# Performance work log

Hardware: AMD Instinct MI355X
Metric: run time of the kernel (lower is better)

Reference implementation:

```python
import jax, jax.numpy as jnp
import numpy as np

K_GF = 8      # neighbors used by graph filtering
EPS = 1e-5    # BatchNorm eps
B, CW, SD, M = 32, 512, 16, 2048


def _conv1x1(x, w, b):
    # x: [B, Cin, M], w: [Cout, Cin], b: [Cout]
    return jnp.einsum('oi,bim->bom', w, x) + b[None, :, None]


def _bn(x, g, be):
    # training-mode BatchNorm1d over (batch, points)
    mu = jnp.mean(x, axis=(0, 2), keepdims=True)
    var = jnp.var(x, axis=(0, 2), keepdims=True)
    return g[None, :, None] * (x - mu) * jax.lax.rsqrt(var + EPS) + be[None, :, None]


def _graph_filtering(x):
    # x: [B, 3, M]  -> sharpening filter over kNN graph: out = 2*x - mean(neighbors)
    pts = jnp.transpose(x, (0, 2, 1))                      # [B, M, 3]
    sq = jnp.sum(pts * pts, axis=-1)                       # [B, M]
    d = sq[:, :, None] + sq[:, None, :] - 2.0 * jnp.einsum('bmc,bnc->bmn', pts, pts)
    idx = jax.lax.top_k(-d, K_GF + 1)[1][..., 1:]          # [B, M, K] drop self
    neigh = jax.vmap(lambda p, i: p[i])(pts, idx)          # [B, M, K, 3]
    out = 2.0 * pts - jnp.mean(neigh, axis=2)
    return jnp.transpose(out, (0, 2, 1))


def setup_inputs() -> dict:
    key = jax.random.key(0)
    ks = jax.random.split(key, 12)
    def w(k, o, i):
        return jax.random.normal(k, (o, i), jnp.float32) * (1.0 / np.sqrt(i))
    h = [256, CW, 512, 256, 128, 64]
    inp = {
        'z': jax.random.normal(ks[0], (B, CW), jnp.float32),
        's': jax.random.normal(ks[1], (B, SD, M), jnp.float32),
        'w_m1': w(ks[2], h[0], SD), 'b_m1': jnp.zeros((h[0],), jnp.float32),
        'w_m2': w(ks[3], h[1], h[0]), 'b_m2': jnp.zeros((h[1],), jnp.float32),
        'w_out': w(ks[4], 3, h[5]), 'b_out': jnp.zeros((3,), jnp.float32),
    }
    for j, (ci, co) in enumerate(zip(h[1:-1], h[2:])):
        inp[f'w_c{j}'] = w(ks[5 + j], co, ci)
        inp[f'b_c{j}'] = jnp.zeros((co,), jnp.float32)
        inp[f'g_c{j}'] = jnp.ones((co,), jnp.float32)
        inp[f'be_c{j}'] = jnp.zeros((co,), jnp.float32)
    return inp


def reference(z, s, w_m1, b_m1, w_m2, b_m2, w_out, b_out,
              w_c0, b_c0, g_c0, be_c0, w_c1, b_c1, g_c1, be_c1,
              w_c2, b_c2, g_c2, be_c2, w_c3, b_c3, g_c3, be_c3):
    x = s / jnp.linalg.norm(s, axis=1, keepdims=True)          # unit samples
    x = jax.nn.relu(_conv1x1(x, w_m1, b_m1))                   # map_samples1
    x = jnp.clip(_conv1x1(x, w_m2, b_m2), -1.0, 1.0)           # map_samples2 (Hardtanh)
    x = z[:, :, None] * x                                      # z-modulation
    for w_, b_, g_, be_ in ((w_c0, b_c0, g_c0, be_c0), (w_c1, b_c1, g_c1, be_c1),
                            (w_c2, b_c2, g_c2, be_c2), (w_c3, b_c3, g_c3, be_c3)):
        x = jax.nn.relu(_bn(_conv1x1(x, w_, b_), g_, be_))
    x = _conv1x1(x, w_out, b_out)                              # [B, 3, M]
    return _graph_filtering(x)
```

## Files before the change

kernel.cpp:

```cpp
#include <hip/hip_runtime.h>
#include <math.h>

#define Bn 32
#define Mn 2048
#define Nn 65536
#define Hn 32768
#define SDn 16
#define CWn 512
#define EPSf 1e-5f
#define KGF 8
#define WTOT 573440
#define LSC 2048.0f
#define LSCI (1.0f / 2048.0f)

typedef unsigned short u16;
typedef _Float16 fp16_t;
typedef __attribute__((ext_vector_type(8))) _Float16 h8v;
typedef __attribute__((ext_vector_type(4))) float f4v;

__device__ __forceinline__ u16 f2h(float f) {
    union { fp16_t h; u16 u; } c; c.h = (fp16_t)f; return c.u;
}
__device__ __forceinline__ float h2f(u16 u) {
    union { fp16_t h; u16 u; } c; c.u = u; return (float)c.h;
}
__device__ __forceinline__ void fsplit(float f, u16& hi, u16& lo) {
    hi = f2h(f);
    lo = f2h((f - h2f(hi)) * LSC);
}
__device__ __forceinline__ float fjoin(u16 hi, u16 lo) {
    return h2f(hi) + h2f(lo) * LSCI;
}
__device__ __forceinline__ void gll16(const u16* g, u16* l) {
    __builtin_amdgcn_global_load_lds((const __attribute__((address_space(1))) void*)g,
                                     (__attribute__((address_space(3))) void*)l, 16, 0, 0);
}
__device__ __forceinline__ unsigned umin(unsigned a, unsigned b) { return a < b ? a : b; }
__device__ __forceinline__ unsigned umax(unsigned a, unsigned b) { return a > b ? a : b; }

__global__ __launch_bounds__(256) void prep_kernel(
    const float* __restrict__ wm1, const float* __restrict__ wm2,
    const float* __restrict__ wc0, const float* __restrict__ wc1,
    const float* __restrict__ wc2, const float* __restrict__ wc3,
    const float* __restrict__ s,
    u16* __restrict__ wbuf, u16* __restrict__ xs, float* __restrict__ stats)
{
    const int bid = blockIdx.x;
    const int tid = threadIdx.x;
    if (bid < 2240) {
        int i = bid * 256 + tid;
        float w; int r, k, Cin; size_t base;
        if (i < 8192) {
            r = i >> 5; k = i & 31; Cin = 32; base = 0;
            w = (k < SDn) ? wm1[r * SDn + k] : 0.f;
        } else {
            int j = i - 8192;
            if (j < 131072)                    { r = j >> 8; k = j & 255; Cin = 256; base = 16384;   w = wm2[j]; }
            else if ((j -= 131072) < 262144)   { r = j >> 9; k = j & 511; Cin = 512; base = 278528;  w = wc0[j]; }
            else if ((j -= 262144) < 131072)   { r = j >> 9; k = j & 511; Cin = 512; base = 802816;  w = wc1[j]; }
            else if ((j -= 131072) < 32768)    { r = j >> 8; k = j & 255; Cin = 256; base = 1064960; w = wc2[j]; }
            else { j -= 32768;                   r = j >> 7; k = j & 127; Cin = 128; base = 1130496; w = wc3[j]; }
        }
        const size_t addr = base + (size_t)r * (2 * Cin) + k;
        u16 hi, lo; fsplit(w, hi, lo);
        wbuf[addr] = hi;
        wbuf[addr + Cin] = lo;
    } else if (bid < 2496) {
        const int b2 = bid - 2240;
        const int m = (b2 & 7) * 256 + tid;
        const int b = b2 >> 3;
        const float* sp = s + (size_t)b * SDn * Mn + m;
        float v[SDn]; float sq = 0.f;
#pragma unroll
        for (int c = 0; c < SDn; ++c) { v[c] = sp[(size_t)c * Mn]; sq += v[c] * v[c]; }
        const float r = 1.0f / sqrtf(sq);
        unsigned int uh[8], ul[8];
#pragma unroll
        for (int c = 0; c < 8; ++c) {
            u16 h0, l0, h1, l1;
            fsplit(v[2 * c] * r, h0, l0);
            fsplit(v[2 * c + 1] * r, h1, l1);
            uh[c] = (unsigned int)h0 | ((unsigned int)h1 << 16);
            ul[c] = (unsigned int)l0 | ((unsigned int)l1 << 16);
        }
        uint4* xp = (uint4*)(xs + (size_t)(b * Mn + m) * 64);
        xp[0] = make_uint4(uh[0], uh[1], uh[2], uh[3]);
        xp[1] = make_uint4(uh[4], uh[5], uh[6], uh[7]);
        xp[2] = make_uint4(0, 0, 0, 0);
        xp[3] = make_uint4(0, 0, 0, 0);
        xp[4] = make_uint4(ul[0], ul[1], ul[2], ul[3]);
        xp[5] = make_uint4(ul[4], ul[5], ul[6], ul[7]);
        xp[6] = make_uint4(0, 0, 0, 0);
        xp[7] = make_uint4(0, 0, 0, 0);
    } else {
        float4 z4 = {0.f, 0.f, 0.f, 0.f};
        float4* sp4 = (float4*)stats;
#pragma unroll
        for (int k = 0; k < 4; ++k) sp4[tid * 4 + k] = z4;
    }
}

template<int RW, int CWv, int EPI, int MY, int IBN, int CINT, int NT>
__global__ __launch_bounds__(NT) void mfma_gemm(
    const u16* __restrict__ W, const u16* __restrict__ X, u16* __restrict__ Y,
    const float* __restrict__ bias, const float* __restrict__ zmod,
    const float* __restrict__ statsIn, const float* __restrict__ gin,
    const float* __restrict__ bein, float* __restrict__ stats, int Cout)
{
    static_assert(NT == RW * CWv * 64, "wave grid must exactly cover the tile");
    constexpr int BM = RW * 64, BN = CWv * 64;
    constexpr int ASEG = (BM * 4) / NT;
    constexpr int BSEG = (BN * 4) / NT;
    constexpr int LMY = (MY == 1) ? 0 : (MY == 2) ? 1 : (MY == 4) ? 2 : 3;
    constexpr int SW = 2 * CINT;
    constexpr int NST = CINT >> 5;
    constexpr int VMSTEP = 2 * ASEG + 2 * BSEG;
    constexpr int SSTATN = (EPI == 2) ? (CWv * BM * 2) : 1;
    constexpr int BNN = IBN ? (CINT * 2) : 1;
    constexpr int AUXN = (SSTATN > BNN) ? SSTATN : BNN;
    constexpr int BSTR = 2 * BM + 8;
    constexpr int BROWS = CWv * 16;
    constexpr int UNITS = BROWS * 2 * (BM / 8);
    static_assert(UNITS % NT == 0, "store units must tile the block");
    __shared__ __align__(16) u16 Ah[2][BM * 32], Al[2][BM * 32];
    __shared__ __align__(16) u16 Bh[2][BN * 32], Bl[2][BN * 32];
    __shared__ __align__(16) u16 bounce[BROWS * BSTR];
    __shared__ float saux[AUXN];

    const int tid = threadIdx.x;
    const int wave = tid >> 6;
    const int lane = tid & 63;
    const int wm = wave & (RW - 1), wn = wave / RW;
    const int l15 = lane & 15, q = lane >> 4;
    const int lin = blockIdx.x;
    const int xcd = lin & 7;
    const int jj = lin >> 3;
    const int m0 = (jj & (MY - 1)) * BM;
    const int n0 = (xcd + ((jj >> LMY) << 3)) * BN;

    f4v acc0[4][4], accL[4][4];
#pragma unroll
    for (int i = 0; i < 4; ++i)
#pragma unroll
        for (int j = 0; j < 4; ++j) {
            acc0[i][j] = (f4v){0.f, 0.f, 0.f, 0.f};
            accL[i][j] = (f4v){0.f, 0.f, 0.f, 0.f};
        }

    auto stageAB = [&](int ks, int buf) {
        const int k0 = ks << 5;
#pragma unroll
        for (int s = 0; s < ASEG; ++s) {
            const int flat = s * NT + tid;
            const int row = flat >> 2;
            const int qs = (flat & 3) ^ ((row >> 1) & 3);
            const u16* ga = W + (size_t)(m0 + row) * SW + k0 + qs * 8;
            gll16(ga, Ah[buf] + flat * 8);
            gll16(ga + CINT, Al[buf] + flat * 8);
        }
#pragma unroll
        for (int s = 0; s < BSEG; ++s) {
            const int flat = s * NT + tid;
            const int row = flat >> 2;
            const int qs = (flat & 3) ^ ((row >> 1) & 3);
            const u16* gb = X + (size_t)(n0 + row) * SW + k0 + qs * 8;
            gll16(gb, Bh[buf] + flat * 8);
            gll16(gb + CINT, Bl[buf] + flat * 8);
        }
    };

    if constexpr (IBN) {
        const float inv = 1.0f / (float)Nn;
        for (int c = tid; c < CINT; c += NT) {
            const float mean = statsIn[c * 2] * inv;
            const float var = statsIn[c * 2 + 1] * inv - mean * mean;
            const float sc = gin[c] / sqrtf(var + EPSf);
            saux[c * 2] = sc;
            saux[c * 2 + 1] = fmaf(-mean, sc, bein[c]);
        }
        asm volatile("s_waitcnt vmcnt(0) lgkmcnt(0)" ::: "memory");
    }
    stageAB(0, 0);
    if constexpr (NST > 1) stageAB(1, 1);

#pragma unroll 1
    for (int ks = 0; ks < NST; ++ks) {
        const int cur = ks & 1;
        if (ks + 1 < NST) {
            asm volatile("s_waitcnt vmcnt(%0)" :: "n"(VMSTEP) : "memory");
        } else {
            asm volatile("s_waitcnt vmcnt(0)" ::: "memory");
        }
        __builtin_amdgcn_s_barrier();
        __builtin_amdgcn_sched_barrier(0);
        h8v afh[4], afl[4], bfh[4], bfl[4];
#pragma unroll
        for (int i = 0; i < 4; ++i) {
            const int ar = wm * 64 + i * 16 + l15;
            const int ao = ar * 32 + ((q ^ ((ar >> 1) & 3)) << 3);
            afh[i] = *(const h8v*)(Ah[cur] + ao);
            afl[i] = *(const h8v*)(Al[cur] + ao);
        }
#pragma unroll
        for (int j = 0; j < 4; ++j) {
            const int br = wn * 64 + j * 16 + l15;
            const int bo = br * 32 + ((q ^ ((br >> 1) & 3)) << 3);
            bfh[j] = *(const h8v*)(Bh[cur] + bo);
            bfl[j] = *(const h8v*)(Bl[cur] + bo);
        }
        if constexpr (IBN) {
            const int kb = ((ks << 5) + q * 8) * 2;
            const float4 p0 = *(const float4*)(saux + kb);
            const float4 p1 = *(const float4*)(saux + kb + 4);
            const float4 p2 = *(const float4*)(saux + kb + 8);
            const float4 p3 = *(const float4*)(saux + kb + 12);
            const float sc8[8] = {p0.x, p0.z, p1.x, p1.z, p2.x, p2.z, p3.x, p3.z};
            const float sh8[8] = {p0.y, p0.w, p1.y, p1.w, p2.y, p2.w, p3.y, p3.w};
#pragma unroll
            for (int j = 0; j < 4; ++j) {
#pragma unroll
                for (int e = 0; e < 8; ++e) {
                    const float v = (float)bfh[j][e] + (float)bfl[j][e] * LSCI;
                    const float a = fmaxf(fmaf(v, sc8[e], sh8[e]), 0.f);
                    const fp16_t hh = (fp16_t)a;
                    bfh[j][e] = hh;
                    bfl[j][e] = (fp16_t)((a - (float)hh) * LSC);
                }
            }
        }
        __builtin_amdgcn_s_setprio(1);
#pragma unroll
        for (int i = 0; i < 4; ++i)
#pragma unroll
            for (int j = 0; j < 4; ++j)
                accL[i][j] = __builtin_amdgcn_mfma_f32_16x16x32_f16(afh[i], bfl[j], accL[i][j], 0, 0, 0);
#pragma unroll
        for (int i = 0; i < 4; ++i)
#pragma unroll
            for (int j = 0; j < 4; ++j)
                acc0[i][j] = __builtin_amdgcn_mfma_f32_16x16x32_f16(afh[i], bfh[j], acc0[i][j], 0, 0, 0);
#pragma unroll
        for (int i = 0; i < 4; ++i)
#pragma unroll
            for (int j = 0; j < 4; ++j)
                accL[i][j] = __builtin_amdgcn_mfma_f32_16x16x32_f16(afl[i], bfh[j], accL[i][j], 0, 0, 0);
        __builtin_amdgcn_s_setprio(0);
        __builtin_amdgcn_s_barrier();
        if (ks + 2 < NST) stageAB(ks + 2, cur);
    }

    float* sstat = saux;
    const int bb = n0 >> 11;
    const int SY = 2 * Cout;
    float ssum[4][4], ssq[4][4];
    if constexpr (EPI == 2) {
#pragma unroll
        for (int i = 0; i < 4; ++i)
#pragma unroll
            for (int r = 0; r < 4; ++r) { ssum[i][r] = 0.f; ssq[i][r] = 0.f; }
    }
    const int nl_w = wn * 16 + l15;
#pragma unroll
    for (int j = 0; j < 4; ++j) {
        __builtin_amdgcn_s_barrier();
#pragma unroll
        for (int i = 0; i < 4; ++i) {
            const int chb = m0 + wm * 64 + i * 16 + q * 4;
            const float4 bias4 = *(const float4*)(bias + chb);
            float v0 = fmaf(accL[i][j][0], LSCI, acc0[i][j][0]) + bias4.x;
            float v1 = fmaf(accL[i][j][1], LSCI, acc0[i][j][1]) + bias4.y;
            float v2 = fmaf(accL[i][j][2], LSCI, acc0[i][j][2]) + bias4.z;
            float v3 = fmaf(accL[i][j][3], LSCI, acc0[i][j][3]) + bias4.w;
            if constexpr (EPI == 0) {
                v0 = fmaxf(v0, 0.f); v1 = fmaxf(v1, 0.f); v2 = fmaxf(v2, 0.f); v3 = fmaxf(v3, 0.f);
            } else if constexpr (EPI == 1) {
                const float4 z4 = *(const float4*)(zmod + bb * CWn + chb);
                v0 = fminf(fmaxf(v0, -1.f), 1.f) * z4.x;
                v1 = fminf(fmaxf(v1, -1.f), 1.f) * z4.y;
                v2 = fminf(fmaxf(v2, -1.f), 1.f) * z4.z;
                v3 = fminf(fmaxf(v3, -1.f), 1.f) * z4.w;
            } else {
                ssum[i][0] += v0; ssum[i][1] += v1; ssum[i][2] += v2; ssum[i][3] += v3;
                ssq[i][0] += v0 * v0; ssq[i][1] += v1 * v1; ssq[i][2] += v2 * v2; ssq[i][3] += v3 * v3;
            }
            u16 h0, l0, h1, l1, h2, l2, h3, l3;
            fsplit(v0, h0, l0); fsplit(v1, h1, l1);
            fsplit(v2, h2, l2); fsplit(v3, h3, l3);
            const ushort4 hv = {h0, h1, h2, h3};
            const ushort4 lv = {l0, l1, l2, l3};
            const int chl = wm * 64 + i * 16 + q * 4;
            *(ushort4*)(bounce + nl_w * BSTR + chl) = hv;
            *(ushort4*)(bounce + nl_w * BSTR + BM + chl) = lv;
        }
        __builtin_amdgcn_s_barrier();
#pragma unroll
        for (int u0 = 0; u0 < UNITS; u0 += NT) {
            const int u = u0 + tid;
            const int nl = u / (2 * (BM / 8));
            const int rem = u % (2 * (BM / 8));
            const int plane = rem / (BM / 8);
            const int off8 = rem % (BM / 8);
            const int n = n0 + (nl >> 4) * 64 + j * 16 + (nl & 15);
            u16* yp = Y + (size_t)n * SY + (plane ? Cout : 0) + m0 + off8 * 8;
            *(uint4*)yp = *(const uint4*)(bounce + nl * BSTR + plane * BM + off8 * 8);
        }
    }
    if constexpr (EPI == 2) {
#pragma unroll
        for (int i = 0; i < 4; ++i) {
#pragma unroll
            for (int r = 0; r < 4; ++r) {
#pragma unroll
                for (int d = 1; d < 16; d <<= 1) {
                    ssum[i][r] += __shfl_xor(ssum[i][r], d);
                    ssq[i][r]  += __shfl_xor(ssq[i][r], d);
                }
            }
            if (l15 == 0) {
                const int chl = wm * 64 + i * 16 + q * 4;
#pragma unroll
                for (int r = 0; r < 4; ++r) {
                    sstat[(wn * BM + chl + r) * 2]     = ssum[i][r];
                    sstat[(wn * BM + chl + r) * 2 + 1] = ssq[i][r];
                }
            }
        }
        __syncthreads();
        if (tid < BM) {
            float s0 = 0.f, s1 = 0.f;
#pragma unroll
            for (int w = 0; w < CWv; ++w) {
                s0 += sstat[(w * BM + tid) * 2];
                s1 += sstat[(w * BM + tid) * 2 + 1];
            }
            atomicAdd(&stats[(m0 + tid) * 2], s0);
            atomicAdd(&stats[(m0 + tid) * 2 + 1], s1);
        }
    }
}

__global__ __launch_bounds__(256) void finalconv_pm(
    const u16* __restrict__ y3, const float* __restrict__ statsIn,
    const float* __restrict__ gin, const float* __restrict__ bein,
    const float* __restrict__ wout, const float* __restrict__ bout,
    float* __restrict__ pts)
{
    __shared__ float swo[3][64];
    __shared__ float ssc[64], ssh[64];
    const int tid = threadIdx.x;
    if (tid < 192) swo[tid / 64][tid % 64] = wout[tid];
    if (tid < 64) {
        const float inv = 1.0f / (float)Nn;
        const float mean = statsIn[tid * 2] * inv;
        const float var = statsIn[tid * 2 + 1] * inv - mean * mean;
        const float sc = gin[tid] / sqrtf(var + EPSf);
        ssc[tid] = sc;
        ssh[tid] = fmaf(-mean, sc, bein[tid]);
    }
    __syncthreads();
    const int n = blockIdx.x * 256 + tid;
    const uint4* yph = (const uint4*)(y3 + (size_t)n * 128);
    float d0 = bout[0], d1 = bout[1], d2 = bout[2];
#pragma unroll
    for (int cc = 0; cc < 8; ++cc) {
        const uint4 H = yph[cc];
        const uint4 L = yph[8 + cc];
        const unsigned hu[4] = {H.x, H.y, H.z, H.w};
        const unsigned lu[4] = {L.x, L.y, L.z, L.w};
#pragma unroll
        for (int e = 0; e < 4; ++e) {
            const int c = cc * 8 + e * 2;
            const float v0 = fjoin((u16)(hu[e] & 0xffff), (u16)(lu[e] & 0xffff));
            const float v1 = fjoin((u16)(hu[e] >> 16), (u16)(lu[e] >> 16));
            const float a0 = fmaxf(fmaf(v0, ssc[c], ssh[c]), 0.f);
            const float a1 = fmaxf(fmaf(v1, ssc[c + 1], ssh[c + 1]), 0.f);
            d0 = fmaf(a0, swo[0][c], d0); d0 = fmaf(a1, swo[0][c + 1], d0);
            d1 = fmaf(a0, swo[1][c], d1); d1 = fmaf(a1, swo[1][c + 1], d1);
            d2 = fmaf(a0, swo[2][c], d2); d2 = fmaf(a1, swo[2][c + 1], d2);
        }
    }
    float4 p = {d0, d1, d2, d0 * d0 + d1 * d1 + d2 * d2};
    *(float4*)(pts + (size_t)n * 4) = p;
}

__global__ __launch_bounds__(512) void knn_kernel(const float* __restrict__ pts,
                                                  float* __restrict__ out) {
    __shared__ __align__(16) float4 sp[Mn];
    const int b = blockIdx.y;
    const int tid = threadIdx.x;
    const float4* pb = (const float4*)pts + (size_t)b * Mn;
    for (int i = tid; i < Mn; i += 512) sp[i] = pb[i];
    __syncthreads();
    const int lane = tid & 63;
    const int wv = tid >> 6;
    const int seg = lane & 15;
    const int ptl = (wv << 2) | (lane >> 4);
    const int m = blockIdx.x * 32 + ptl;
    const float4 p = sp[m];
    const int cself = (seg == (m >> 7)) ? (m & 127) : 128;
    const int nb = seg << 7;
    unsigned bk[8];
#pragma unroll
    for (int k = 0; k < 8; ++k) bk[k] = 0xFFFFFFFFu;
    for (int t = 0; t < 128; ++t) {
        const int tt = (t + seg) & 127;
        const float4 q = sp[nb | tt];
        const float dot = fmaf(p.x, q.x, fmaf(p.y, q.y, p.z * q.z));
        float d = fmaf(-2.f, dot, q.w + p.w);
        d = fmaxf(d, 0.f);
        unsigned key = (__float_as_uint(d) & 0xFFFFFF80u) | (unsigned)tt;
        key = (tt == cself) ? 0xFFFFFFFFu : key;
        bk[7] = umin(bk[7], key);
#pragma unroll
        for (int k = 6; k >= 0; --k) {
            const unsigned lo = umin(bk[k], bk[k + 1]);
            bk[k + 1] = umax(bk[k], bk[k + 1]);
            bk[k] = lo;
        }
    }
    unsigned ok[8];
#pragma unroll
    for (int k = 0; k < 8; ++k) ok[k] = bk[k];
#pragma unroll
    for (int r = 1; r <= 8; r <<= 1) {
        unsigned od[8], md[8];
#pragma unroll
        for (int k = 0; k < 8; ++k) od[k] = (unsigned)__shfl_xor((int)bk[k], r);
#pragma unroll
        for (int k = 0; k < 8; ++k) md[k] = umin(bk[k], od[7 - k]);
#define CSU(a, c) { const unsigned lo_ = umin(md[a], md[c]); md[c] = umax(md[a], md[c]); md[a] = lo_; }
        CSU(0,4); CSU(1,5); CSU(2,6); CSU(3,7);
        CSU(0,2); CSU(1,3); CSU(4,6); CSU(5,7);
        CSU(0,1); CSU(2,3); CSU(4,5); CSU(6,7);
#undef CSU
#pragma unroll
        for (int k = 0; k < 8; ++k) bk[k] = md[k];
    }
    const unsigned TK = bk[7];
    float slt[4] = {0.f, 0.f, 0.f, 0.f};
    float seq[4] = {0.f, 0.f, 0.f, 0.f};
#pragma unroll
    for (int k = 0; k < 8; ++k) {
        const unsigned key = ok[k];
        const float4 q = sp[nb | (int)(key & 127u)];
        const bool lt = key < TK;
        const bool eq = key == TK;
        slt[0] += lt ? q.x : 0.f; slt[1] += lt ? q.y : 0.f;
        slt[2] += lt ? q.z : 0.f; slt[3] += lt ? 1.f : 0.f;
        seq[0] += eq ? q.x : 0.f; seq[1] += eq ? q.y : 0.f;
        seq[2] += eq ? q.z : 0.f; seq[3] += eq ? 1.f : 0.f;
    }
#pragma unroll
    for (int r = 1; r <= 8; r <<= 1) {
#pragma unroll
        for (int k = 0; k < 4; ++k) {
            slt[k] += __shfl_xor(slt[k], r);
            seq[k] += __shfl_xor(seq[k], r);
        }
    }
    if (seg == 0) {
        const float scale = (8.f - slt[3]) / seq[3];
        const float nx = fmaf(scale, seq[0], slt[0]);
        const float ny = fmaf(scale, seq[1], slt[1]);
        const float nz = fmaf(scale, seq[2], slt[2]);
        const float s8 = 0.125f;
        float* ob = out + (size_t)b * 3 * Mn;
        ob[m]          = 2.f * p.x - nx * s8;
        ob[Mn + m]     = 2.f * p.y - ny * s8;
        ob[2 * Mn + m] = 2.f * p.z - nz * s8;
    }
}

extern "C" void kernel_launch(void* const* d_in, const int* in_sizes, int n_in,
                              void* d_out, int out_size, void* d_ws, size_t ws_size,
                              hipStream_t stream)
{
    (void)in_sizes; (void)n_in; (void)out_size;
    const float* z     = (const float*)d_in[0];
    const float* s     = (const float*)d_in[1];
    const float* w_m1  = (const float*)d_in[2];
    const float* b_m1  = (const float*)d_in[3];
    const float* w_m2  = (const float*)d_in[4];
    const float* b_m2  = (const float*)d_in[5];
    const float* w_out = (const float*)d_in[6];
    const float* b_out = (const float*)d_in[7];
    const float* w_c[4]  = {(const float*)d_in[8],  (const float*)d_in[12], (const float*)d_in[16], (const float*)d_in[20]};
    const float* b_c[4]  = {(const float*)d_in[9],  (const float*)d_in[13], (const float*)d_in[17], (const float*)d_in[21]};
    const float* g_c[4]  = {(const float*)d_in[10], (const float*)d_in[14], (const float*)d_in[18], (const float*)d_in[22]};
    const float* be_c[4] = {(const float*)d_in[11], (const float*)d_in[15], (const float*)d_in[19], (const float*)d_in[23]};

    char* ws = (char*)d_ws;
    const size_t MB = 1024ull * 1024ull;
    float* outp = (float*)d_out;
    if (ws_size < 208 * MB) return;

    u16*   wbuf  = (u16*)ws;
    float* stats = (float*)(ws + 3 * MB);
    u16*   xs  = (u16*)(ws + 4 * MB);
    u16*   x1  = (u16*)(ws + 12 * MB);
    u16*   x2  = (u16*)(ws + 76 * MB);
    u16*   y0  = (u16*)(ws + 12 * MB);
    u16*   y0a = (u16*)(ws + 12 * MB);
    u16*   y0b = (u16*)(ws + 76 * MB);
    u16*   y1  = (u16*)(ws + 140 * MB);
    u16*   y2  = (u16*)(ws + 12 * MB);
    u16*   y3  = (u16*)(ws + 76 * MB);
    float* pts = (float*)(ws + 4 * MB);

    prep_kernel<<<2497, 256, 0, stream>>>(w_m1, w_m2, w_c[0], w_c[1], w_c[2], w_c[3], s, wbuf, xs, stats);
    mfma_gemm<2, 2, 0, 2, 0, 32, 256><<<1024, 256, 0, stream>>>(wbuf, xs, x1, b_m1, nullptr, nullptr, nullptr, nullptr, nullptr, 256);
    mfma_gemm<4, 2, 1, 2, 0, 256, 512><<<1024, 512, 0, stream>>>(wbuf + 16384, x1, x2, b_m2, z, nullptr, nullptr, nullptr, nullptr, 512);
    mfma_gemm<4, 2, 2, 2, 0, 512, 512><<<512, 512, 0, stream>>>(wbuf + 278528, x2, y0a, b_c[0], nullptr, nullptr, nullptr, nullptr, stats + 0, 512);
    mfma_gemm<4, 2, 2, 2, 0, 512, 512><<<512, 512, 0, stream>>>(wbuf + 278528, x2 + (size_t)Hn * 1024, y0b, b_c[0], nullptr, nullptr, nullptr, nullptr, stats + 0, 512);
    mfma_gemm<4, 2, 2, 1, 1, 512, 512><<<512, 512, 0, stream>>>(wbuf + 802816, y0, y1, b_c[1], nullptr, stats + 0, g_c[0], be_c[0], stats + 1024, 256);
    mfma_gemm<2, 4, 2, 1, 1, 256, 512><<<256, 512, 0, stream>>>(wbuf + 1064960, y1, y2, b_c[2], nullptr, stats + 1024, g_c[1], be_c[1], stats + 2048, 128);
    mfma_gemm<1, 4, 2, 1, 1, 128, 256><<<256, 256, 0, stream>>>(wbuf + 1130496, y2, y3, b_c[3], nullptr, stats + 2048, g_c[2], be_c[2], stats + 3072, 64);
    finalconv_pm<<<Nn / 256, 256, 0, stream>>>(y3, stats + 3072, g_c[3], be_c[3], w_out, b_out, pts);
    knn_kernel<<<dim3(Mn / 32, Bn), 512, 0, stream>>>(pts, outp);
}
```

Measured before the change: 537.9 us.

## Deepen B-operand prefetch pipeline to four stages and alias epilogue LDS

Splits A and B staging into separate functions so the B (activation) tiles can be prefetched up to four k-steps ahead, while the A (weight) tiles stay double-buffered. The vmcnt wait counts are adjusted to match. To make room in LDS, the epilogue bounce buffer and stats scratch now alias the staging buffers inside one unified shared array. The goal is to hide more global-load latency in the large GEMMs, at the cost of more LDS per block, which may limit occupancy.

```diff
diff --git a/kernel.cpp b/kernel.cpp
--- a/kernel.cpp
+++ b/kernel.cpp
@@ -100,7 +100,7 @@
     }
 }
 
-template<int RW, int CWv, int EPI, int MY, int IBN, int CINT, int NT>
+template<int RW, int CWv, int EPI, int MY, int IBN, int CINT, int NT, int BD>
 __global__ __launch_bounds__(NT) void mfma_gemm(
     const u16* __restrict__ W, const u16* __restrict__ X, u16* __restrict__ Y,
     const float* __restrict__ bias, const float* __restrict__ zmod,
@@ -108,24 +108,31 @@
     const float* __restrict__ bein, float* __restrict__ stats, int Cout)
 {
     static_assert(NT == RW * CWv * 64, "wave grid must exactly cover the tile");
+    static_assert(BD == 2 || BD == 4, "B depth must be 2 or 4");
     constexpr int BM = RW * 64, BN = CWv * 64;
     constexpr int ASEG = (BM * 4) / NT;
     constexpr int BSEG = (BN * 4) / NT;
+    constexpr int ASTEP = 2 * ASEG;
+    constexpr int BSTEP = 2 * BSEG;
     constexpr int LMY = (MY == 1) ? 0 : (MY == 2) ? 1 : (MY == 4) ? 2 : 3;
     constexpr int SW = 2 * CINT;
     constexpr int NST = CINT >> 5;
-    constexpr int VMSTEP = 2 * ASEG + 2 * BSEG;
-    constexpr int SSTATN = (EPI == 2) ? (CWv * BM * 2) : 1;
-    constexpr int BNN = IBN ? (CINT * 2) : 1;
-    constexpr int AUXN = (SSTATN > BNN) ? SSTATN : BNN;
     constexpr int BSTR = 2 * BM + 8;
     constexpr int BROWS = CWv * 16;
     constexpr int UNITS = BROWS * 2 * (BM / 8);
     static_assert(UNITS % NT == 0, "store units must tile the block");
-    __shared__ __align__(16) u16 Ah[2][BM * 32], Al[2][BM * 32];
-    __shared__ __align__(16) u16 Bh[2][BN * 32], Bl[2][BN * 32];
-    __shared__ __align__(16) u16 bounce[BROWS * BSTR];
-    __shared__ float saux[AUXN];
+    constexpr int ABYTES = BM * 256;
+    constexpr int BBYTES = BN * 128 * BD;
+    constexpr int SAUXB  = IBN ? (CINT * 8) : 16;
+    constexpr int BOUNCEB = BROWS * BSTR * 2;
+    constexpr int SSTATB = (EPI == 2) ? (CWv * BM * 2 * 4) : 16;
+    static_assert(BOUNCEB + 16 + SSTATB <= ABYTES + BBYTES, "alias overflow");
+    __shared__ __align__(16) char smem[ABYTES + BBYTES + SAUXB];
+    u16* const AhB = (u16*)smem;
+    u16* const AlB = AhB + 2 * BM * 32;
+    u16* const BhB = AlB + 2 * BM * 32;
+    u16* const BlB = BhB + BD * BN * 32;
+    float* const saux = (float*)(smem + ABYTES + BBYTES);
 
     const int tid = threadIdx.x;
     const int wave = tid >> 6;
@@ -147,25 +154,32 @@
             accL[i][j] = (f4v){0.f, 0.f, 0.f, 0.f};
         }
 
-    auto stageAB = [&](int ks, int buf) {
+    auto stageA = [&](int ks, int abuf) {
         const int k0 = ks << 5;
+        u16* const ah = AhB + abuf * BM * 32;
+        u16* const al = AlB + abuf * BM * 32;
 #pragma unroll
         for (int s = 0; s < ASEG; ++s) {
             const int flat = s * NT + tid;
             const int row = flat >> 2;
             const int qs = (flat & 3) ^ ((row >> 1) & 3);
             const u16* ga = W + (size_t)(m0 + row) * SW + k0 + qs * 8;
-            gll16(ga, Ah[buf] + flat * 8);
-            gll16(ga + CINT, Al[buf] + flat * 8);
-        }
+            gll16(ga, ah + flat * 8);
+            gll16(ga + CINT, al + flat * 8);
+        }
+    };
+    auto stageB = [&](int ks, int bbuf) {
+        const int k0 = ks << 5;
+        u16* const bh = BhB + bbuf * BN * 32;
+        u16* const bl = BlB + bbuf * BN * 32;
 #pragma unroll
         for (int s = 0; s < BSEG; ++s) {
             const int flat = s * NT + tid;
             const int row = flat >> 2;
             const int qs = (flat & 3) ^ ((row >> 1) & 3);
             const u16* gb = X + (size_t)(n0 + row) * SW + k0 + qs * 8;
-            gll16(gb, Bh[buf] + flat * 8);
-            gll16(gb + CINT, Bl[buf] + flat * 8);
+            gll16(gb, bh + flat * 8);
+            gll16(gb + CINT, bl + flat * 8);
         }
     };
 
@@ -180,33 +194,45 @@
         }
         asm volatile("s_waitcnt vmcnt(0) lgkmcnt(0)" ::: "memory");
     }
-    stageAB(0, 0);
-    if constexpr (NST > 1) stageAB(1, 1);
+    stageA(0, 0);
+    stageB(0, 0);
+    if constexpr (NST > 1) { stageA(1, 1); stageB(1, 1); }
+    if constexpr (BD > 2 && NST > 2) stageB(2, 2);
+    if constexpr (BD > 3 && NST > 3) stageB(3, 3);
 
 #pragma unroll 1
     for (int ks = 0; ks < NST; ++ks) {
-        const int cur = ks & 1;
-        if (ks + 1 < NST) {
-            asm volatile("s_waitcnt vmcnt(%0)" :: "n"(VMSTEP) : "memory");
+        const int acur = ks & 1;
+        const int bcur = ks & (BD - 1);
+        if (BD >= 4 && ks + 3 < NST) {
+            asm volatile("s_waitcnt vmcnt(%0)" :: "n"(ASTEP + 3 * BSTEP) : "memory");
+        } else if (BD >= 3 && ks + 2 < NST) {
+            asm volatile("s_waitcnt vmcnt(%0)" :: "n"(ASTEP + 2 * BSTEP) : "memory");
+        } else if (ks + 1 < NST) {
+            asm volatile("s_waitcnt vmcnt(%0)" :: "n"(ASTEP + BSTEP) : "memory");
         } else {
             asm volatile("s_waitcnt vmcnt(0)" ::: "memory");
         }
         __builtin_amdgcn_s_barrier();
         __builtin_amdgcn_sched_barrier(0);
         h8v afh[4], afl[4], bfh[4], bfl[4];
+        const u16* const ahc = AhB + acur * BM * 32;
+        const u16* const alc = AlB + acur * BM * 32;
+        const u16* const bhc = BhB + bcur * BN * 32;
+        const u16* const blc = BlB + bcur * BN * 32;
 #pragma unroll
         for (int i = 0; i < 4; ++i) {
             const int ar = wm * 64 + i * 16 + l15;
             const int ao = ar * 32 + ((q ^ ((ar >> 1) & 3)) << 3);
-            afh[i] = *(const h8v*)(Ah[cur] + ao);
-            afl[i] = *(const h8v*)(Al[cur] + ao);
+            afh[i] = *(const h8v*)(ahc + ao);
+            afl[i] = *(const h8v*)(alc + ao);
         }
 #pragma unroll
         for (int j = 0; j < 4; ++j) {
             const int br = wn * 64 + j * 16 + l15;
             const int bo = br * 32 + ((q ^ ((br >> 1) & 3)) << 3);
-            bfh[j] = *(const h8v*)(Bh[cur] + bo);
-            bfl[j] = *(const h8v*)(Bl[cur] + bo);
+            bfh[j] = *(const h8v*)(bhc + bo);
+            bfl[j] = *(const h8v*)(blc + bo);
         }
         if constexpr (IBN) {
             const int kb = ((ks << 5) + q * 8) * 2;
@@ -246,10 +272,12 @@
                 accL[i][j] = __builtin_amdgcn_mfma_f32_16x16x32_f16(afl[i], bfh[j], accL[i][j], 0, 0, 0);
         __builtin_amdgcn_s_setprio(0);
         __builtin_amdgcn_s_barrier();
-        if (ks + 2 < NST) stageAB(ks + 2, cur);
-    }
-
-    float* sstat = saux;
+        if (ks + 2 < NST) stageA(ks + 2, (ks + 2) & 1);
+        if (ks + BD < NST) stageB(ks + BD, bcur);
+    }
+
+    u16* const bounce = (u16*)smem;
+    float* const sstat = (float*)(smem + ((BOUNCEB + 15) & ~15));
     const int bb = n0 >> 11;
     const int SY = 2 * Cout;
     float ssum[4][4], ssq[4][4];
@@ -508,13 +536,13 @@
     float* pts = (float*)(ws + 4 * MB);
 
     prep_kernel<<<2497, 256, 0, stream>>>(w_m1, w_m2, w_c[0], w_c[1], w_c[2], w_c[3], s, wbuf, xs, stats);
-    mfma_gemm<2, 2, 0, 2, 0, 32, 256><<<1024, 256, 0, stream>>>(wbuf, xs, x1, b_m1, nullptr, nullptr, nullptr, nullptr, nullptr, 256);
-    mfma_gemm<4, 2, 1, 2, 0, 256, 512><<<1024, 512, 0, stream>>>(wbuf + 16384, x1, x2, b_m2, z, nullptr, nullptr, nullptr, nullptr, 512);
-    mfma_gemm<4, 2, 2, 2, 0, 512, 512><<<512, 512, 0, stream>>>(wbuf + 278528, x2, y0a, b_c[0], nullptr, nullptr, nullptr, nullptr, stats + 0, 512);
-    mfma_gemm<4, 2, 2, 2, 0, 512, 512><<<512, 512, 0, stream>>>(wbuf + 278528, x2 + (size_t)Hn * 1024, y0b, b_c[0], nullptr, nullptr, nullptr, nullptr, stats + 0, 512);
-    mfma_gemm<4, 2, 2, 1, 1, 512, 512><<<512, 512, 0, stream>>>(wbuf + 802816, y0, y1, b_c[1], nullptr, stats + 0, g_c[0], be_c[0], stats + 1024, 256);
-    mfma_gemm<2, 4, 2, 1, 1, 256, 512><<<256, 512, 0, stream>>>(wbuf + 1064960, y1, y2, b_c[2], nullptr, stats + 1024, g_c[1], be_c[1], stats + 2048, 128);
-    mfma_gemm<1, 4, 2, 1, 1, 128, 256><<<256, 256, 0, stream>>>(wbuf + 1130496, y2, y3, b_c[3], nullptr, stats + 2048, g_c[2], be_c[2], stats + 3072, 64);
+    mfma_gemm<2, 2, 0, 2, 0, 32, 256, 2><<<1024, 256, 0, stream>>>(wbuf, xs, x1, b_m1, nullptr, nullptr, nullptr, nullptr, nullptr, 256);
+    mfma_gemm<4, 2, 1, 2, 0, 256, 512, 4><<<1024, 512, 0, stream>>>(wbuf + 16384, x1, x2, b_m2, z, nullptr, nullptr, nullptr, nullptr, 512);
+    mfma_gemm<4, 2, 2, 2, 0, 512, 512, 4><<<512, 512, 0, stream>>>(wbuf + 278528, x2, y0a, b_c[0], nullptr, nullptr, nullptr, nullptr, stats + 0, 512);
+    mfma_gemm<4, 2, 2, 2, 0, 512, 512, 4><<<512, 512, 0, stream>>>(wbuf + 278528, x2 + (size_t)Hn * 1024, y0b, b_c[0], nullptr, nullptr, nullptr, nullptr, stats + 0, 512);
+    mfma_gemm<4, 2, 2, 1, 1, 512, 512, 4><<<512, 512, 0, stream>>>(wbuf + 802816, y0, y1, b_c[1], nullptr, stats + 0, g_c[0], be_c[0], stats + 1024, 256);
+    mfma_gemm<2, 4, 2, 1, 1, 256, 512, 2><<<256, 512, 0, stream>>>(wbuf + 1064960, y1, y2, b_c[2], nullptr, stats + 1024, g_c[1], be_c[1], stats + 2048, 128);
+    mfma_gemm<1, 4, 2, 1, 1, 128, 256, 2><<<256, 256, 0, stream>>>(wbuf + 1130496, y2, y3, b_c[3], nullptr, stats + 2048, g_c[2], be_c[2], stats + 3072, 64);
     finalconv_pm<<<Nn / 256, 256, 0, stream>>>(y3, stats + 3072, g_c[3], be_c[3], w_out, b_out, pts);
     knn_kernel<<<dim3(Mn / 32, Bn), 512, 0, stream>>>(pts, outp);
 }
```

Measured after the change: 541.6 us. About the same (+0.7%).

## Triple-buffer GEMM LDS staging and drop trailing per-iteration barrier

Applied to the files above, without the earlier changes.

Moves the MFMA GEMM K-loop from double to triple buffering in one flat LDS array. The prefetch for step ks+2 now goes out right after the top-of-loop barrier instead of after a second barrier at the loop end, which cuts one barrier per K-step and lets loads overlap more with compute. The epilogue bounce and stat buffers now alias the staging area to limit the LDS growth. The larger LDS footprint may lower occupancy, and the aliasing relies on all staging traffic being finished before the epilogue.

```diff
diff --git a/kernel.cpp b/kernel.cpp
--- a/kernel.cpp
+++ b/kernel.cpp
@@ -111,21 +111,28 @@
     constexpr int BM = RW * 64, BN = CWv * 64;
     constexpr int ASEG = (BM * 4) / NT;
     constexpr int BSEG = (BN * 4) / NT;
+    constexpr int STEP = 2 * ASEG + 2 * BSEG;
     constexpr int LMY = (MY == 1) ? 0 : (MY == 2) ? 1 : (MY == 4) ? 2 : 3;
     constexpr int SW = 2 * CINT;
     constexpr int NST = CINT >> 5;
-    constexpr int VMSTEP = 2 * ASEG + 2 * BSEG;
-    constexpr int SSTATN = (EPI == 2) ? (CWv * BM * 2) : 1;
-    constexpr int BNN = IBN ? (CINT * 2) : 1;
-    constexpr int AUXN = (SSTATN > BNN) ? SSTATN : BNN;
     constexpr int BSTR = 2 * BM + 8;
     constexpr int BROWS = CWv * 16;
     constexpr int UNITS = BROWS * 2 * (BM / 8);
     static_assert(UNITS % NT == 0, "store units must tile the block");
-    __shared__ __align__(16) u16 Ah[2][BM * 32], Al[2][BM * 32];
-    __shared__ __align__(16) u16 Bh[2][BN * 32], Bl[2][BN * 32];
-    __shared__ __align__(16) u16 bounce[BROWS * BSTR];
-    __shared__ float saux[AUXN];
+    constexpr int APLANE = BM * 32;
+    constexpr int BPLANE = BN * 32;
+    constexpr int STAGEB = 3 * (APLANE + BPLANE) * 2 * 2;
+    constexpr int SAUXB  = IBN ? (CINT * 8) : 16;
+    constexpr int BOUNCEB = BROWS * BSTR * 2;
+    constexpr int SSTATB = (EPI == 2) ? (CWv * BM * 2 * 4) : 16;
+    static_assert(BOUNCEB + 16 + SSTATB <= STAGEB, "alias overflow");
+    static_assert(STAGEB + SAUXB <= 160 * 1024, "LDS overflow");
+    __shared__ __align__(16) char smem[STAGEB + SAUXB];
+    u16* const AhB = (u16*)smem;
+    u16* const AlB = AhB + 3 * APLANE;
+    u16* const BhB = AlB + 3 * APLANE;
+    u16* const BlB = BhB + 3 * BPLANE;
+    float* const saux = (float*)(smem + STAGEB);
 
     const int tid = threadIdx.x;
     const int wave = tid >> 6;
@@ -147,16 +154,21 @@
             accL[i][j] = (f4v){0.f, 0.f, 0.f, 0.f};
         }
 
-    auto stageAB = [&](int ks, int buf) {
+    auto stage = [&](int ks) {
+        const int slot = ks % 3;
         const int k0 = ks << 5;
+        u16* const ah = AhB + slot * APLANE;
+        u16* const al = AlB + slot * APLANE;
+        u16* const bh = BhB + slot * BPLANE;
+        u16* const bl = BlB + slot * BPLANE;
 #pragma unroll
         for (int s = 0; s < ASEG; ++s) {
             const int flat = s * NT + tid;
             const int row = flat >> 2;
             const int qs = (flat & 3) ^ ((row >> 1) & 3);
             const u16* ga = W + (size_t)(m0 + row) * SW + k0 + qs * 8;
-            gll16(ga, Ah[buf] + flat * 8);
-            gll16(ga + CINT, Al[buf] + flat * 8);
+            gll16(ga, ah + flat * 8);
+            gll16(ga + CINT, al + flat * 8);
         }
 #pragma unroll
         for (int s = 0; s < BSEG; ++s) {
@@ -164,8 +176,8 @@
             const int row = flat >> 2;
             const int qs = (flat & 3) ^ ((row >> 1) & 3);
             const u16* gb = X + (size_t)(n0 + row) * SW + k0 + qs * 8;
-            gll16(gb, Bh[buf] + flat * 8);
-            gll16(gb + CINT, Bl[buf] + flat * 8);
+            gll16(gb, bh + flat * 8);
+            gll16(gb + CINT, bl + flat * 8);
         }
     };
 
@@ -180,33 +192,38 @@
         }
         asm volatile("s_waitcnt vmcnt(0) lgkmcnt(0)" ::: "memory");
     }
-    stageAB(0, 0);
-    if constexpr (NST > 1) stageAB(1, 1);
+    stage(0);
+    if constexpr (NST > 1) stage(1);
 
 #pragma unroll 1
     for (int ks = 0; ks < NST; ++ks) {
-        const int cur = ks & 1;
+        const int slot = ks % 3;
         if (ks + 1 < NST) {
-            asm volatile("s_waitcnt vmcnt(%0)" :: "n"(VMSTEP) : "memory");
+            asm volatile("s_waitcnt vmcnt(%0)" :: "n"(STEP) : "memory");
         } else {
             asm volatile("s_waitcnt vmcnt(0)" ::: "memory");
         }
         __builtin_amdgcn_s_barrier();
         __builtin_amdgcn_sched_barrier(0);
+        if (ks + 2 < NST) stage(ks + 2);
         h8v afh[4], afl[4], bfh[4], bfl[4];
+        const u16* const ahc = AhB + slot * APLANE;
+        const u16* const alc = AlB + slot * APLANE;
+        const u16* const bhc = BhB + slot * BPLANE;
+        const u16* const blc = BlB + slot * BPLANE;
 #pragma unroll
         for (int i = 0; i < 4; ++i) {
             const int ar = wm * 64 + i * 16 + l15;
             const int ao = ar * 32 + ((q ^ ((ar >> 1) & 3)) << 3);
-            afh[i] = *(const h8v*)(Ah[cur] + ao);
-            afl[i] = *(const h8v*)(Al[cur] + ao);
+            afh[i] = *(const h8v*)(ahc + ao);
+            afl[i] = *(const h8v*)(alc + ao);
         }
 #pragma unroll
         for (int j = 0; j < 4; ++j) {
             const int br = wn * 64 + j * 16 + l15;
             const int bo = br * 32 + ((q ^ ((br >> 1) & 3)) << 3);
-            bfh[j] = *(const h8v*)(Bh[cur] + bo);
-            bfl[j] = *(const h8v*)(Bl[cur] + bo);
+            bfh[j] = *(const h8v*)(bhc + bo);
+            bfl[j] = *(const h8v*)(blc + bo);
         }
         if constexpr (IBN) {
             const int kb = ((ks << 5) + q * 8) * 2;
@@ -245,11 +262,10 @@
             for (int j = 0; j < 4; ++j)
                 accL[i][j] = __builtin_amdgcn_mfma_f32_16x16x32_f16(afl[i], bfh[j], accL[i][j], 0, 0, 0);
         __builtin_amdgcn_s_setprio(0);
-        __builtin_amdgcn_s_barrier();
-        if (ks + 2 < NST) stageAB(ks + 2, cur);
-    }
-
-    float* sstat = saux;
+    }
+
+    u16* const bounce = (u16*)smem;
+    float* const sstat = (float*)(smem + ((BOUNCEB + 15) & ~15));
     const int bb = n0 >> 11;
     const int SY = 2 * Cout;
     float ssum[4][4], ssq[4][4];
```

Measured after the change: 555.5 us. +3.3%, slower.
